# Kernel tuning notes

Hardware: AMD Instinct MI355X
Metric: run time of the kernel (lower is better)

Reference implementation:

```python
import jax, jax.numpy as jnp
import numpy as np

B, S, H, NH = 2, 2048, 1024, 16
HD = H // NH  # 64


def setup_inputs() -> dict:
    key = jax.random.key(0)
    ks = jax.random.split(key, 11)
    sc = 1.0 / np.sqrt(H)
    inp = {
        "q": jax.random.normal(ks[0], (B, S, H), dtype=jnp.float32),
        "k": jax.random.normal(ks[1], (B, S, H), dtype=jnp.float32),
        "v": jax.random.normal(ks[2], (B, S, H), dtype=jnp.float32),
        # nn.Linear params: weight [out,in], bias [out]
        "wq_w": jax.random.normal(ks[3], (H, H), dtype=jnp.float32) * sc,
        "wq_b": jnp.zeros((H,), dtype=jnp.float32),
        "wk_w": jax.random.normal(ks[4], (H, H), dtype=jnp.float32) * sc,
        "wk_b": jnp.zeros((H,), dtype=jnp.float32),
        "wv_w": jax.random.normal(ks[5], (H, H), dtype=jnp.float32) * sc,
        "wv_b": jnp.zeros((H,), dtype=jnp.float32),
        "wo_w": jax.random.normal(ks[6], (H, H), dtype=jnp.float32) * sc,
        "wo_b": jnp.zeros((H,), dtype=jnp.float32),
    }
    return inp


def _split_heads(x):
    # [B,S,H] -> [B,NH,S,HD]
    b, s, _ = x.shape
    return x.reshape(b, s, NH, HD).transpose(0, 2, 1, 3)


def reference(q, k, v, wq_w, wq_b, wk_w, wk_b, wv_w, wv_b, wo_w, wo_b):
    qw = q @ wq_w.T + wq_b
    kw = k @ wk_w.T + wk_b
    vw = v @ wv_w.T + wv_b
    hq = _split_heads(qw)  # [B,NH,S,HD]
    hk = _split_heads(kw)
    hv = _split_heads(vw)
    scale = 1.0 / jnp.sqrt(jnp.float32(HD))
    scores = jnp.einsum("bhqd,bhkd->bhqk", hq, hk) * scale  # [B,NH,S,S]
    attn = jax.nn.softmax(scores, axis=-1)
    out = jnp.einsum("bhqk,bhkd->bhqd", attn, hv)  # [B,NH,S,HD]
    out = out.transpose(0, 2, 1, 3).reshape(q.shape[0], -1, H)  # [B,S,H]
    final = out @ wo_w.T + wo_b
    return final, attn
```

## Files before the change

### kernel.cpp

```cpp
#include <hip/hip_runtime.h>

typedef short bf16x8 __attribute__((ext_vector_type(8)));
typedef float f32x4 __attribute__((ext_vector_type(4)));
typedef unsigned short ushort4v __attribute__((ext_vector_type(4)));
typedef unsigned short ushort8 __attribute__((ext_vector_type(8)));

#define DEVI static __device__ __forceinline__

DEVI unsigned short f2bf(float f) {
    unsigned u = __float_as_uint(f);
    u += 0x7FFFu + ((u >> 16) & 1u);
    return (unsigned short)(u >> 16);
}

DEVI unsigned cvtpk(float lo, float hi) {
    unsigned r;
    asm("v_cvt_pk_bf16_f32 %0, %1, %2" : "=v"(r) : "v"(lo), "v"(hi));
    return r;
}

typedef __attribute__((address_space(3))) unsigned int* lds_ptr_t;
typedef const __attribute__((address_space(1))) unsigned int* gbl_ptr_t;
#define GLDS(gp, lp) __builtin_amdgcn_global_load_lds((gbl_ptr_t)(gp), (lds_ptr_t)(lp), 16, 0, 0)

__global__ void cvt_kernel(const float* __restrict__ src, unsigned short* __restrict__ dst, int n) {
    int i = (blockIdx.x * 256 + threadIdx.x) * 4;
    if (i >= n) return;
    float4 v = *(const float4*)(src + i);
    ushort4v o;
    o.x = f2bf(v.x); o.y = f2bf(v.y); o.z = f2bf(v.z); o.w = f2bf(v.w);
    *(ushort4v*)(dst + i) = o;
}

__global__ void cvt2_kernel(const float* __restrict__ s0, unsigned short* __restrict__ d0, int n0,
                            const float* __restrict__ s1, unsigned short* __restrict__ d1, int n1) {
    int idx = blockIdx.x * 256 + threadIdx.x;
    const int c0 = n0 >> 2;
    const float* src; unsigned short* dst; int i;
    if (idx < c0) { src = s0; dst = d0; i = idx * 4; }
    else {
        i = (idx - c0) * 4;
        if (i >= n1) return;
        src = s1; dst = d1;
    }
    float4 v = *(const float4*)(src + i);
    ushort4v o;
    o.x = f2bf(v.x); o.y = f2bf(v.y); o.z = f2bf(v.z); o.w = f2bf(v.w);
    *(ushort4v*)(dst + i) = o;
}

__global__ void cvt4_kernel(const float* __restrict__ q, const float* __restrict__ k,
                            const float* __restrict__ v, const float* __restrict__ wq,
                            const float* __restrict__ wk, const float* __restrict__ wv,
                            const float* __restrict__ wo, unsigned short* __restrict__ dq,
                            unsigned short* __restrict__ dk, unsigned short* __restrict__ dv,
                            unsigned short* __restrict__ dwq, unsigned short* __restrict__ dwk,
                            unsigned short* __restrict__ dwv, unsigned short* __restrict__ dwo) {
    int idx = blockIdx.x * 256 + threadIdx.x;
    const float* src; unsigned short* dst; int base;
    if (idx < 1048576) { src = q; dst = dq; base = idx; }
    else if (idx < 2097152) { src = k; dst = dk; base = idx - 1048576; }
    else if (idx < 3145728) { src = v; dst = dv; base = idx - 2097152; }
    else if (idx < 3407872) { src = wq; dst = dwq; base = idx - 3145728; }
    else if (idx < 3670016) { src = wk; dst = dwk; base = idx - 3407872; }
    else if (idx < 3932160) { src = wv; dst = dwv; base = idx - 3670016; }
    else { src = wo; dst = dwo; base = idx - 3932160; }
    const int i = base * 4;
    float4 x = *(const float4*)(src + i);
    ushort4v o;
    o.x = f2bf(x.x); o.y = f2bf(x.y); o.z = f2bf(x.z); o.w = f2bf(x.w);
    *(ushort4v*)(dst + i) = o;
}

#define GEMM_BODY(A, W)                                                                             \
    constexpr int K = 1024;                                                                         \
    __shared__ unsigned short Asb[2][64 * 32];                                                      \
    __shared__ unsigned short Bsb[2][128 * 32];                                                     \
    const int t = threadIdx.x;                                                                      \
    const int w = t >> 6, l = t & 63;                                                               \
    const int wr = w >> 1, wc = w & 1;                                                              \
    const int fr = l & 15, fg = l >> 4;                                                             \
    const int m0 = blockIdx.y * 64, n0 = blockIdx.x * 128;                                          \
    const int ra = t >> 2, qa = (t & 3) * 8;                                                        \
    const int c1 = 256 + t, rb1 = c1 >> 2, qb1 = (c1 & 3) * 8;                                      \
    f32x4 acc[2][4] = {};                                                                           \
    GLDS(A + (size_t)(m0 + ra) * K + qa, &Asb[0][t * 8]);                                           \
    GLDS(W + (size_t)(n0 + ra) * K + qa, &Bsb[0][t * 8]);                                           \
    GLDS(W + (size_t)(n0 + rb1) * K + qb1, &Bsb[0][c1 * 8]);                                        \
    for (int t2 = 0; t2 < 32; ++t2) {                                                               \
        const int cur = t2 & 1;                                                                     \
        if (t2 < 31) {                                                                              \
            const int kb = (t2 + 1) * 32;                                                           \
            GLDS(A + (size_t)(m0 + ra) * K + kb + qa, &Asb[cur ^ 1][t * 8]);                        \
            GLDS(W + (size_t)(n0 + ra) * K + kb + qa, &Bsb[cur ^ 1][t * 8]);                        \
            GLDS(W + (size_t)(n0 + rb1) * K + kb + qb1, &Bsb[cur ^ 1][c1 * 8]);                     \
            asm volatile("s_waitcnt vmcnt(3)" ::: "memory");                                        \
        } else {                                                                                    \
            asm volatile("s_waitcnt vmcnt(0)" ::: "memory");                                        \
        }                                                                                           \
        __syncthreads();                                                                            \
        bf16x8 af[2], bfv[4];                                                                       \
        _Pragma("unroll") for (int mi = 0; mi < 2; mi++)                                            \
            af[mi] = *(const bf16x8*)(&Asb[cur][(wr * 32 + mi * 16 + fr) * 32 + fg * 8]);           \
        _Pragma("unroll") for (int ni = 0; ni < 4; ni++)                                            \
            bfv[ni] = *(const bf16x8*)(&Bsb[cur][(wc * 64 + ni * 16 + fr) * 32 + fg * 8]);          \
        _Pragma("unroll") for (int mi = 0; mi < 2; mi++)                                            \
            _Pragma("unroll") for (int ni = 0; ni < 4; ni++)                                        \
                acc[mi][ni] = __builtin_amdgcn_mfma_f32_16x16x32_bf16(af[mi], bfv[ni], acc[mi][ni], 0, 0, 0); \
        __syncthreads();                                                                            \
    }

template <int MODE>
__global__ __launch_bounds__(256) void gemm_bt(const unsigned short* __restrict__ A,
                                               const unsigned short* __restrict__ W,
                                               const float* __restrict__ bias,
                                               void* __restrict__ Cout) {
    GEMM_BODY(A, W)
#pragma unroll
    for (int ni = 0; ni < 4; ni++) {
        const int n = n0 + wc * 64 + ni * 16 + fr;
        const float bv = bias[n];
#pragma unroll
        for (int mi = 0; mi < 2; mi++) {
            const int mb = m0 + wr * 32 + mi * 16 + fg * 4;
            if constexpr (MODE == 1) {
                float* C = (float*)Cout;
#pragma unroll
                for (int r = 0; r < 4; r++) C[(size_t)(mb + r) * 1024 + n] = acc[mi][ni][r] + bv;
            } else if constexpr (MODE == 0) {
                unsigned short* C = (unsigned short*)Cout;
                const int h = n >> 6, hd = n & 63;
#pragma unroll
                for (int r = 0; r < 4; r++) {
                    const int m = mb + r;
                    const int bb = m >> 11, s = m & 2047;
                    C[(size_t)((bb * 16 + h) * 2048 + s) * 64 + hd] = f2bf(acc[mi][ni][r] + bv);
                }
            } else {
                unsigned short* C = (unsigned short*)Cout;
                const int h = n >> 6, hd = n & 63;
                const int bb = mb >> 11, s = mb & 2047;
                const int blk = s >> 6, off = s & 63;
                const int pos = blk * 64 + (off >> 5) * 32 + ((off & 15) >> 2) * 8 + ((off >> 4) & 1) * 4;
                ushort4v pk;
                pk.x = f2bf(acc[mi][ni][0] + bv);
                pk.y = f2bf(acc[mi][ni][1] + bv);
                pk.z = f2bf(acc[mi][ni][2] + bv);
                pk.w = f2bf(acc[mi][ni][3] + bv);
                *(ushort4v*)(C + (size_t)((bb * 16 + h) * 64 + hd) * 2048 + pos) = pk;
            }
        }
    }
}

__global__ __launch_bounds__(256) void gemm_qkv(const unsigned short* __restrict__ Aq,
                                                const unsigned short* __restrict__ Ak,
                                                const unsigned short* __restrict__ Av,
                                                const unsigned short* __restrict__ Wq,
                                                const unsigned short* __restrict__ Wk,
                                                const unsigned short* __restrict__ Wv,
                                                const float* __restrict__ bq,
                                                const float* __restrict__ bk,
                                                const float* __restrict__ bv_,
                                                unsigned short* __restrict__ qh,
                                                unsigned short* __restrict__ kh,
                                                unsigned short* __restrict__ vt) {
    constexpr int K = 1024;
    __shared__ unsigned short Asb[2][128 * 32];
    __shared__ unsigned short Bsb[2][128 * 32];
    const int z = blockIdx.z;
    const unsigned short* A = (z == 0) ? Aq : (z == 1) ? Ak : Av;
    const unsigned short* W = (z == 0) ? Wq : (z == 1) ? Wk : Wv;
    const float* bias = (z == 0) ? bq : (z == 1) ? bk : bv_;

    const int t = threadIdx.x;
    const int w = t >> 6, l = t & 63;
    const int wr = w >> 1, wc = w & 1;
    const int fr = l & 15, fg = l >> 4;
    const int m0 = blockIdx.y * 128, n0 = blockIdx.x * 128;

    const int c0 = t, c1 = 256 + t;
    const int r0 = c0 >> 2, q0off = (c0 & 3) * 8;
    const int r1 = c1 >> 2, q1off = (c1 & 3) * 8;

    f32x4 acc[4][4] = {};

#define STG128(kb, pb)                                                        \
    {                                                                         \
        GLDS(A + (size_t)(m0 + r0) * K + (kb) + q0off, &Asb[pb][c0 * 8]);     \
        GLDS(A + (size_t)(m0 + r1) * K + (kb) + q1off, &Asb[pb][c1 * 8]);     \
        GLDS(W + (size_t)(n0 + r0) * K + (kb) + q0off, &Bsb[pb][c0 * 8]);     \
        GLDS(W + (size_t)(n0 + r1) * K + (kb) + q1off, &Bsb[pb][c1 * 8]);     \
    }

    STG128(0, 0);
    for (int t2 = 0; t2 < 32; ++t2) {
        const int cur = t2 & 1;
        if (t2 < 31) {
            STG128((t2 + 1) * 32, cur ^ 1);
            asm volatile("s_waitcnt vmcnt(4)" ::: "memory");
        } else {
            asm volatile("s_waitcnt vmcnt(0)" ::: "memory");
        }
        __syncthreads();
        bf16x8 af[4], bfv[4];
#pragma unroll
        for (int mi = 0; mi < 4; mi++)
            af[mi] = *(const bf16x8*)(&Asb[cur][(wr * 64 + mi * 16 + fr) * 32 + fg * 8]);
#pragma unroll
        for (int ni = 0; ni < 4; ni++)
            bfv[ni] = *(const bf16x8*)(&Bsb[cur][(wc * 64 + ni * 16 + fr) * 32 + fg * 8]);
#pragma unroll
        for (int mi = 0; mi < 4; mi++)
#pragma unroll
            for (int ni = 0; ni < 4; ni++)
                acc[mi][ni] = __builtin_amdgcn_mfma_f32_16x16x32_bf16(af[mi], bfv[ni], acc[mi][ni], 0, 0, 0);
        __syncthreads();
    }
#undef STG128

#pragma unroll
    for (int ni = 0; ni < 4; ni++) {
        const int n = n0 + wc * 64 + ni * 16 + fr;
        const float bv = bias[n];
        const int h = n >> 6, hd = n & 63;
#pragma unroll
        for (int mi = 0; mi < 4; mi++) {
            const int mb = m0 + wr * 64 + mi * 16 + fg * 4;
            if (z == 2) {
                const int bb = mb >> 11, s = mb & 2047;
                const int blk = s >> 6, off = s & 63;
                const int pos = blk * 64 + (off >> 5) * 32 + ((off & 15) >> 2) * 8 + ((off >> 4) & 1) * 4;
                ushort4v pk;
                pk.x = f2bf(acc[mi][ni][0] + bv);
                pk.y = f2bf(acc[mi][ni][1] + bv);
                pk.z = f2bf(acc[mi][ni][2] + bv);
                pk.w = f2bf(acc[mi][ni][3] + bv);
                *(ushort4v*)(vt + (size_t)((bb * 16 + h) * 64 + hd) * 2048 + pos) = pk;
            } else {
                unsigned short* C = (z == 0) ? qh : kh;
#pragma unroll
                for (int r = 0; r < 4; r++) {
                    const int m = mb + r;
                    const int bb = m >> 11, s = m & 2047;
                    C[(size_t)((bb * 16 + h) * 2048 + s) * 64 + hd] = f2bf(acc[mi][ni][r] + bv);
                }
            }
        }
    }
}

__global__ __launch_bounds__(256, 2) void attn_kernel(const unsigned short* __restrict__ Qh,
                                                      const unsigned short* __restrict__ Kh,
                                                      const unsigned short* __restrict__ Vt,
                                                      unsigned short* __restrict__ Obuf,
                                                      float* __restrict__ AttnOut) {
    __shared__ float rpart[32][4];
    __shared__ float rinv_s[32];
    __shared__ float ored[32][68];

    const int i = blockIdx.x;
    const int qt = i & 63, bh = i >> 6;
    const int b = bh >> 4, h = bh & 15;
    const int q0 = qt * 32;
    const int t = threadIdx.x, w = t >> 6, l = t & 63;
    const int fr = l & 15, fg = l >> 4;
    const float SCL = 0.1803368801111f;

    const unsigned short* qb = Qh + (size_t)(bh * 2048 + q0) * 64;
    bf16x8 qf[2][2];
#pragma unroll
    for (int qs = 0; qs < 2; qs++)
#pragma unroll
        for (int kc = 0; kc < 2; kc++)
            qf[qs][kc] = *(const bf16x8*)(qb + (size_t)(qs * 16 + fr) * 64 + kc * 32 + fg * 8);

    const unsigned short* kbase = Kh + ((size_t)bh * 2048 + w * 512) * 64;
    const unsigned short* vtb = Vt + (size_t)bh * 64 * 2048;

    unsigned p0[8][8], p1[8][8];
    float rs0 = 0.f, rs1 = 0.f;
#pragma unroll
    for (int kt = 0; kt < 8; ++kt) {
#pragma unroll
        for (int mt = 0; mt < 4; ++mt) {
            const unsigned short* kr = kbase + (size_t)(kt * 64 + mt * 16 + fr) * 64 + fg * 8;
            bf16x8 kf0 = *(const bf16x8*)kr;
            bf16x8 kf1 = *(const bf16x8*)(kr + 32);
            f32x4 d0 = {}, d1 = {};
            d0 = __builtin_amdgcn_mfma_f32_16x16x32_bf16(kf0, qf[0][0], d0, 0, 0, 0);
            d0 = __builtin_amdgcn_mfma_f32_16x16x32_bf16(kf1, qf[0][1], d0, 0, 0, 0);
            d1 = __builtin_amdgcn_mfma_f32_16x16x32_bf16(kf0, qf[1][0], d1, 0, 0, 0);
            d1 = __builtin_amdgcn_mfma_f32_16x16x32_bf16(kf1, qf[1][1], d1, 0, 0, 0);
            const float a0 = exp2f(d0[0] * SCL), a1 = exp2f(d0[1] * SCL);
            const float a2 = exp2f(d0[2] * SCL), a3 = exp2f(d0[3] * SCL);
            rs0 += (a0 + a1) + (a2 + a3);
            p0[kt][mt * 2] = cvtpk(a0, a1);
            p0[kt][mt * 2 + 1] = cvtpk(a2, a3);
            const float c0 = exp2f(d1[0] * SCL), c1 = exp2f(d1[1] * SCL);
            const float c2 = exp2f(d1[2] * SCL), c3 = exp2f(d1[3] * SCL);
            rs1 += (c0 + c1) + (c2 + c3);
            p1[kt][mt * 2] = cvtpk(c0, c1);
            p1[kt][mt * 2 + 1] = cvtpk(c2, c3);
        }
    }
    rs0 += __shfl_xor(rs0, 16, 64); rs0 += __shfl_xor(rs0, 32, 64);
    rs1 += __shfl_xor(rs1, 16, 64); rs1 += __shfl_xor(rs1, 32, 64);
    if (l < 16) { rpart[l][w] = rs0; rpart[l + 16][w] = rs1; }
    __syncthreads();
    if (t < 32) rinv_s[t] = 1.0f / (rpart[t][0] + rpart[t][1] + rpart[t][2] + rpart[t][3]);
    __syncthreads();
    const float ri0 = rinv_s[fr], ri1 = rinv_s[16 + fr];

    float* attnB0 = AttnOut + (size_t)bh * 2048 * 2048 + (size_t)(q0 + fr) * 2048 + w * 512;
    float* attnB1 = attnB0 + (size_t)16 * 2048;
    f32x4 opv[2][4] = {};
#pragma unroll
    for (int kt = 0; kt < 8; ++kt) {
        bf16x8 vf[2][4];
#pragma unroll
        for (int kc = 0; kc < 2; ++kc)
#pragma unroll
            for (int dt = 0; dt < 4; ++dt)
                vf[kc][dt] = *(const bf16x8*)(vtb + (size_t)(dt * 16 + fr) * 2048 + w * 512 + kt * 64 + kc * 32 + fg * 8);
#pragma unroll
        for (int mt = 0; mt < 4; ++mt) {
            const unsigned a = p0[kt][mt * 2], aa = p0[kt][mt * 2 + 1];
            f32x4 o;
            o[0] = __uint_as_float(a << 16) * ri0;
            o[1] = __uint_as_float(a & 0xffff0000u) * ri0;
            o[2] = __uint_as_float(aa << 16) * ri0;
            o[3] = __uint_as_float(aa & 0xffff0000u) * ri0;
            __builtin_nontemporal_store(o, (f32x4*)(attnB0 + kt * 64 + mt * 16 + fg * 4));
            const unsigned c = p1[kt][mt * 2], cc = p1[kt][mt * 2 + 1];
            f32x4 o1;
            o1[0] = __uint_as_float(c << 16) * ri1;
            o1[1] = __uint_as_float(c & 0xffff0000u) * ri1;
            o1[2] = __uint_as_float(cc << 16) * ri1;
            o1[3] = __uint_as_float(cc & 0xffff0000u) * ri1;
            __builtin_nontemporal_store(o1, (f32x4*)(attnB1 + kt * 64 + mt * 16 + fg * 4));
        }
#pragma unroll
        for (int kc = 0; kc < 2; ++kc) {
            union { unsigned u[4]; bf16x8 v; } pb0, pb1;
#pragma unroll
            for (int j = 0; j < 4; j++) { pb0.u[j] = p0[kt][4 * kc + j]; pb1.u[j] = p1[kt][4 * kc + j]; }
#pragma unroll
            for (int dt = 0; dt < 4; ++dt) {
                opv[0][dt] = __builtin_amdgcn_mfma_f32_16x16x32_bf16(vf[kc][dt], pb0.v, opv[0][dt], 0, 0, 0);
                opv[1][dt] = __builtin_amdgcn_mfma_f32_16x16x32_bf16(vf[kc][dt], pb1.v, opv[1][dt], 0, 0, 0);
            }
        }
    }

    __syncthreads();
    for (int ww = 0; ww < 4; ++ww) {
        if (w == ww) {
#pragma unroll
            for (int qs = 0; qs < 2; qs++)
#pragma unroll
                for (int dt = 0; dt < 4; dt++)
#pragma unroll
                    for (int r = 0; r < 4; r++) {
                        if (ww == 0)
                            ored[qs * 16 + fr][dt * 16 + 4 * fg + r] = opv[qs][dt][r];
                        else
                            ored[qs * 16 + fr][dt * 16 + 4 * fg + r] += opv[qs][dt][r];
                    }
        }
        __syncthreads();
    }
    {
        const int row = t >> 3, cb = (t & 7) * 8;
        const float rr = rinv_s[row];
        ushort8 pk;
#pragma unroll
        for (int j = 0; j < 8; j++) pk[j] = f2bf(ored[row][cb + j] * rr);
        *(ushort8*)(Obuf + (size_t)(b * 2048 + q0 + row) * 1024 + h * 64 + cb) = pk;
    }
}

extern "C" void kernel_launch(void* const* d_in, const int* in_sizes, int n_in,
                              void* d_out, int out_size, void* d_ws, size_t ws_size,
                              hipStream_t stream) {
    const float* q = (const float*)d_in[0];
    const float* k = (const float*)d_in[1];
    const float* v = (const float*)d_in[2];
    const float* wqw = (const float*)d_in[3];
    const float* wqb = (const float*)d_in[4];
    const float* wkw = (const float*)d_in[5];
    const float* wkb = (const float*)d_in[6];
    const float* wvw = (const float*)d_in[7];
    const float* wvb = (const float*)d_in[8];
    const float* wow = (const float*)d_in[9];
    const float* wob = (const float*)d_in[10];

    float* finalOut = (float*)d_out;
    float* attnOut = finalOut + 4194304;
    char* ws = (char*)d_ws;

    const int NX = 4194304, NW = 1048576;
    dim3 gGrid(8, 64);

    if (ws_size >= 67108864ull) {
        unsigned short* qbf  = (unsigned short*)(ws);
        unsigned short* kbf  = (unsigned short*)(ws + 8388608);
        unsigned short* vbf  = (unsigned short*)(ws + 16777216);
        unsigned short* wqbf = (unsigned short*)(ws + 25165824);
        unsigned short* wkbf = (unsigned short*)(ws + 27262976);
        unsigned short* wvbf = (unsigned short*)(ws + 29360128);
        unsigned short* wobf = (unsigned short*)(ws + 31457280);
        unsigned short* qh   = (unsigned short*)(ws + 33554432);
        unsigned short* kh   = (unsigned short*)(ws + 41943040);
        unsigned short* vt   = (unsigned short*)(ws + 50331648);
        unsigned short* obuf = (unsigned short*)(ws + 58720256);

        cvt4_kernel<<<16384, 256, 0, stream>>>(q, k, v, wqw, wkw, wvw, wow,
                                               qbf, kbf, vbf, wqbf, wkbf, wvbf, wobf);
        dim3 g3(8, 32, 3);
        gemm_qkv<<<g3, 256, 0, stream>>>(qbf, kbf, vbf, wqbf, wkbf, wvbf,
                                         wqb, wkb, wvb, qh, kh, vt);
        attn_kernel<<<2048, 256, 0, stream>>>(qh, kh, vt, obuf, attnOut);
        gemm_bt<1><<<gGrid, 256, 0, stream>>>(obuf, wobf, wob, finalOut);
    } else {
        unsigned short* xbf  = (unsigned short*)(ws);
        unsigned short* wbf  = (unsigned short*)(ws + 8388608);
        unsigned short* qh   = (unsigned short*)(ws + 10485760);
        unsigned short* kh   = (unsigned short*)(ws + 18874368);
        unsigned short* vt   = (unsigned short*)(ws + 27262976);
        unsigned short* obuf = (unsigned short*)(ws + 35651584);
        const int c2grid = (NX + NW) / 1024;

        cvt2_kernel<<<c2grid, 256, 0, stream>>>(q, xbf, NX, wqw, wbf, NW);
        gemm_bt<0><<<gGrid, 256, 0, stream>>>(xbf, wbf, wqb, qh);
        cvt2_kernel<<<c2grid, 256, 0, stream>>>(k, xbf, NX, wkw, wbf, NW);
        gemm_bt<0><<<gGrid, 256, 0, stream>>>(xbf, wbf, wkb, kh);
        cvt2_kernel<<<c2grid, 256, 0, stream>>>(v, xbf, NX, wvw, wbf, NW);
        gemm_bt<2><<<gGrid, 256, 0, stream>>>(xbf, wbf, wvb, vt);
        attn_kernel<<<2048, 256, 0, stream>>>(qh, kh, vt, obuf, attnOut);
        cvt_kernel<<<NW / 1024, 256, 0, stream>>>(wow, wbf, NW);
        gemm_bt<1><<<gGrid, 256, 0, stream>>>(obuf, wbf, wob, finalOut);
    }
}
```

Measured before the change: 269.8 us.

## Split attention block into 8 waves, one 16-query half per wave

```diff
diff --git a/kernel.cpp b/kernel.cpp
--- a/kernel.cpp
+++ b/kernel.cpp
@@ -250,7 +250,7 @@
     }
 }
 
-__global__ __launch_bounds__(256, 2) void attn_kernel(const unsigned short* __restrict__ Qh,
+__global__ __launch_bounds__(512, 4) void attn_kernel(const unsigned short* __restrict__ Qh,
                                                       const unsigned short* __restrict__ Kh,
                                                       const unsigned short* __restrict__ Vt,
                                                       unsigned short* __restrict__ Obuf,
@@ -264,22 +264,21 @@
     const int b = bh >> 4, h = bh & 15;
     const int q0 = qt * 32;
     const int t = threadIdx.x, w = t >> 6, l = t & 63;
+    const int kg = w & 3, qg = w >> 2;
     const int fr = l & 15, fg = l >> 4;
     const float SCL = 0.1803368801111f;
 
-    const unsigned short* qb = Qh + (size_t)(bh * 2048 + q0) * 64;
-    bf16x8 qf[2][2];
-#pragma unroll
-    for (int qs = 0; qs < 2; qs++)
-#pragma unroll
-        for (int kc = 0; kc < 2; kc++)
-            qf[qs][kc] = *(const bf16x8*)(qb + (size_t)(qs * 16 + fr) * 64 + kc * 32 + fg * 8);
-
-    const unsigned short* kbase = Kh + ((size_t)bh * 2048 + w * 512) * 64;
-    const unsigned short* vtb = Vt + (size_t)bh * 64 * 2048;
-
-    unsigned p0[8][8], p1[8][8];
-    float rs0 = 0.f, rs1 = 0.f;
+    const unsigned short* qb = Qh + (size_t)(bh * 2048 + q0 + qg * 16) * 64;
+    bf16x8 qf[2];
+#pragma unroll
+    for (int kc = 0; kc < 2; kc++)
+        qf[kc] = *(const bf16x8*)(qb + (size_t)fr * 64 + kc * 32 + fg * 8);
+
+    const unsigned short* kbase = Kh + ((size_t)bh * 2048 + kg * 512) * 64;
+    const unsigned short* vwb = Vt + (size_t)bh * 64 * 2048 + kg * 512;
+
+    unsigned p[8][8];
+    float rs = 0.f;
 #pragma unroll
     for (int kt = 0; kt < 8; ++kt) {
 #pragma unroll
@@ -287,96 +286,77 @@
             const unsigned short* kr = kbase + (size_t)(kt * 64 + mt * 16 + fr) * 64 + fg * 8;
             bf16x8 kf0 = *(const bf16x8*)kr;
             bf16x8 kf1 = *(const bf16x8*)(kr + 32);
-            f32x4 d0 = {}, d1 = {};
-            d0 = __builtin_amdgcn_mfma_f32_16x16x32_bf16(kf0, qf[0][0], d0, 0, 0, 0);
-            d0 = __builtin_amdgcn_mfma_f32_16x16x32_bf16(kf1, qf[0][1], d0, 0, 0, 0);
-            d1 = __builtin_amdgcn_mfma_f32_16x16x32_bf16(kf0, qf[1][0], d1, 0, 0, 0);
-            d1 = __builtin_amdgcn_mfma_f32_16x16x32_bf16(kf1, qf[1][1], d1, 0, 0, 0);
-            const float a0 = exp2f(d0[0] * SCL), a1 = exp2f(d0[1] * SCL);
-            const float a2 = exp2f(d0[2] * SCL), a3 = exp2f(d0[3] * SCL);
-            rs0 += (a0 + a1) + (a2 + a3);
-            p0[kt][mt * 2] = cvtpk(a0, a1);
-            p0[kt][mt * 2 + 1] = cvtpk(a2, a3);
-            const float c0 = exp2f(d1[0] * SCL), c1 = exp2f(d1[1] * SCL);
-            const float c2 = exp2f(d1[2] * SCL), c3 = exp2f(d1[3] * SCL);
-            rs1 += (c0 + c1) + (c2 + c3);
-            p1[kt][mt * 2] = cvtpk(c0, c1);
-            p1[kt][mt * 2 + 1] = cvtpk(c2, c3);
-        }
-    }
-    rs0 += __shfl_xor(rs0, 16, 64); rs0 += __shfl_xor(rs0, 32, 64);
-    rs1 += __shfl_xor(rs1, 16, 64); rs1 += __shfl_xor(rs1, 32, 64);
-    if (l < 16) { rpart[l][w] = rs0; rpart[l + 16][w] = rs1; }
+            f32x4 d = {};
+            d = __builtin_amdgcn_mfma_f32_16x16x32_bf16(kf0, qf[0], d, 0, 0, 0);
+            d = __builtin_amdgcn_mfma_f32_16x16x32_bf16(kf1, qf[1], d, 0, 0, 0);
+            const float e0 = exp2f(d[0] * SCL), e1 = exp2f(d[1] * SCL);
+            const float e2 = exp2f(d[2] * SCL), e3 = exp2f(d[3] * SCL);
+            rs += (e0 + e1) + (e2 + e3);
+            p[kt][mt * 2] = cvtpk(e0, e1);
+            p[kt][mt * 2 + 1] = cvtpk(e2, e3);
+        }
+    }
+    rs += __shfl_xor(rs, 16, 64);
+    rs += __shfl_xor(rs, 32, 64);
+    if (l < 16) rpart[qg * 16 + l][kg] = rs;
     __syncthreads();
     if (t < 32) rinv_s[t] = 1.0f / (rpart[t][0] + rpart[t][1] + rpart[t][2] + rpart[t][3]);
     __syncthreads();
-    const float ri0 = rinv_s[fr], ri1 = rinv_s[16 + fr];
-
-    float* attnB0 = AttnOut + (size_t)bh * 2048 * 2048 + (size_t)(q0 + fr) * 2048 + w * 512;
-    float* attnB1 = attnB0 + (size_t)16 * 2048;
-    f32x4 opv[2][4] = {};
+    const float ri = rinv_s[qg * 16 + fr];
+
+    float* attnB = AttnOut + (size_t)bh * 2048 * 2048 + (size_t)(q0 + qg * 16 + fr) * 2048 + kg * 512;
+    f32x4 opv[4] = {};
 #pragma unroll
     for (int kt = 0; kt < 8; ++kt) {
-        bf16x8 vf[2][4];
-#pragma unroll
-        for (int kc = 0; kc < 2; ++kc)
+#pragma unroll
+        for (int kc = 0; kc < 2; ++kc) {
+            bf16x8 vf[4];
 #pragma unroll
             for (int dt = 0; dt < 4; ++dt)
-                vf[kc][dt] = *(const bf16x8*)(vtb + (size_t)(dt * 16 + fr) * 2048 + w * 512 + kt * 64 + kc * 32 + fg * 8);
-#pragma unroll
-        for (int mt = 0; mt < 4; ++mt) {
-            const unsigned a = p0[kt][mt * 2], aa = p0[kt][mt * 2 + 1];
-            f32x4 o;
-            o[0] = __uint_as_float(a << 16) * ri0;
-            o[1] = __uint_as_float(a & 0xffff0000u) * ri0;
-            o[2] = __uint_as_float(aa << 16) * ri0;
-            o[3] = __uint_as_float(aa & 0xffff0000u) * ri0;
-            __builtin_nontemporal_store(o, (f32x4*)(attnB0 + kt * 64 + mt * 16 + fg * 4));
-            const unsigned c = p1[kt][mt * 2], cc = p1[kt][mt * 2 + 1];
-            f32x4 o1;
-            o1[0] = __uint_as_float(c << 16) * ri1;
-            o1[1] = __uint_as_float(c & 0xffff0000u) * ri1;
-            o1[2] = __uint_as_float(cc << 16) * ri1;
-            o1[3] = __uint_as_float(cc & 0xffff0000u) * ri1;
-            __builtin_nontemporal_store(o1, (f32x4*)(attnB1 + kt * 64 + mt * 16 + fg * 4));
-        }
-#pragma unroll
-        for (int kc = 0; kc < 2; ++kc) {
-            union { unsigned u[4]; bf16x8 v; } pb0, pb1;
-#pragma unroll
-            for (int j = 0; j < 4; j++) { pb0.u[j] = p0[kt][4 * kc + j]; pb1.u[j] = p1[kt][4 * kc + j]; }
-#pragma unroll
-            for (int dt = 0; dt < 4; ++dt) {
-                opv[0][dt] = __builtin_amdgcn_mfma_f32_16x16x32_bf16(vf[kc][dt], pb0.v, opv[0][dt], 0, 0, 0);
-                opv[1][dt] = __builtin_amdgcn_mfma_f32_16x16x32_bf16(vf[kc][dt], pb1.v, opv[1][dt], 0, 0, 0);
+                vf[dt] = *(const bf16x8*)(vwb + (size_t)(dt * 16 + fr) * 2048 + kt * 64 + kc * 32 + fg * 8);
+            if (kc == 0) {
+#pragma unroll
+                for (int mt = 0; mt < 4; ++mt) {
+                    const unsigned a = p[kt][mt * 2], aa = p[kt][mt * 2 + 1];
+                    f32x4 o;
+                    o[0] = __uint_as_float(a << 16) * ri;
+                    o[1] = __uint_as_float(a & 0xffff0000u) * ri;
+                    o[2] = __uint_as_float(aa << 16) * ri;
+                    o[3] = __uint_as_float(aa & 0xffff0000u) * ri;
+                    __builtin_nontemporal_store(o, (f32x4*)(attnB + kt * 64 + mt * 16 + fg * 4));
+                }
             }
+            union { unsigned u[4]; bf16x8 v; } pb;
+#pragma unroll
+            for (int j = 0; j < 4; j++) pb.u[j] = p[kt][4 * kc + j];
+#pragma unroll
+            for (int dt = 0; dt < 4; ++dt)
+                opv[dt] = __builtin_amdgcn_mfma_f32_16x16x32_bf16(vf[dt], pb.v, opv[dt], 0, 0, 0);
         }
     }
 
     __syncthreads();
     for (int ww = 0; ww < 4; ++ww) {
-        if (w == ww) {
-#pragma unroll
-            for (int qs = 0; qs < 2; qs++)
-#pragma unroll
-                for (int dt = 0; dt < 4; dt++)
-#pragma unroll
-                    for (int r = 0; r < 4; r++) {
-                        if (ww == 0)
-                            ored[qs * 16 + fr][dt * 16 + 4 * fg + r] = opv[qs][dt][r];
-                        else
-                            ored[qs * 16 + fr][dt * 16 + 4 * fg + r] += opv[qs][dt][r];
-                    }
+        if (kg == ww) {
+#pragma unroll
+            for (int dt = 0; dt < 4; dt++)
+#pragma unroll
+                for (int r = 0; r < 4; r++) {
+                    if (ww == 0)
+                        ored[qg * 16 + fr][dt * 16 + 4 * fg + r] = opv[dt][r];
+                    else
+                        ored[qg * 16 + fr][dt * 16 + 4 * fg + r] += opv[dt][r];
+                }
         }
         __syncthreads();
     }
     {
-        const int row = t >> 3, cb = (t & 7) * 8;
+        const int row = t >> 4, cb = (t & 15) * 4;
         const float rr = rinv_s[row];
-        ushort8 pk;
-#pragma unroll
-        for (int j = 0; j < 8; j++) pk[j] = f2bf(ored[row][cb + j] * rr);
-        *(ushort8*)(Obuf + (size_t)(b * 2048 + q0 + row) * 1024 + h * 64 + cb) = pk;
+        ushort4v pk;
+#pragma unroll
+        for (int j = 0; j < 4; j++) pk[j] = f2bf(ored[row][cb + j] * rr);
+        *(ushort4v*)(Obuf + (size_t)(b * 2048 + q0 + row) * 1024 + h * 64 + cb) = pk;
     }
 }
 
@@ -420,7 +400,7 @@
         dim3 g3(8, 32, 3);
         gemm_qkv<<<g3, 256, 0, stream>>>(qbf, kbf, vbf, wqbf, wkbf, wvbf,
                                          wqb, wkb, wvb, qh, kh, vt);
-        attn_kernel<<<2048, 256, 0, stream>>>(qh, kh, vt, obuf, attnOut);
+        attn_kernel<<<2048, 512, 0, stream>>>(qh, kh, vt, obuf, attnOut);
         gemm_bt<1><<<gGrid, 256, 0, stream>>>(obuf, wobf, wob, finalOut);
     } else {
         unsigned short* xbf  = (unsigned short*)(ws);
@@ -437,7 +417,7 @@
         gemm_bt<0><<<gGrid, 256, 0, stream>>>(xbf, wbf, wkb, kh);
         cvt2_kernel<<<c2grid, 256, 0, stream>>>(v, xbf, NX, wvw, wbf, NW);
         gemm_bt<2><<<gGrid, 256, 0, stream>>>(xbf, wbf, wvb, vt);
-        attn_kernel<<<2048, 256, 0, stream>>>(qh, kh, vt, obuf, attnOut);
+        attn_kernel<<<2048, 512, 0, stream>>>(qh, kh, vt, obuf, attnOut);
         cvt_kernel<<<NW / 1024, 256, 0, stream>>>(wow, wbf, NW);
         gemm_bt<1><<<gGrid, 256, 0, stream>>>(obuf, wbf, wob, finalOut);
     }
```

New measurement: 342.5 us. +27.0%, slower.
